# Kernel tuning notes

Measured on AMD Instinct MI355X. Metric: run time of the kernel, lower is better.

## Reference

```python
import jax, jax.numpy as jnp
from jax import lax
import numpy as np

B, T, I, H, L, O = 256, 512, 1, 256, 4, 1


def setup_inputs() -> dict:
    key = jax.random.key(0)
    ks = jax.random.split(key, 4 * L + 3)
    s = 1.0 / np.sqrt(H)
    inp = {"x": jax.random.normal(ks[0], (B, T, I), dtype=jnp.float32)}
    for l in range(L):
        in_dim = I if l == 0 else H
        inp[f"W_ih{l}"] = jax.random.uniform(ks[1 + 4 * l], (4 * H, in_dim), minval=-s, maxval=s, dtype=jnp.float32)
        inp[f"W_hh{l}"] = jax.random.uniform(ks[2 + 4 * l], (4 * H, H), minval=-s, maxval=s, dtype=jnp.float32)
        inp[f"b_ih{l}"] = jax.random.uniform(ks[3 + 4 * l], (4 * H,), minval=-s, maxval=s, dtype=jnp.float32)
        inp[f"b_hh{l}"] = jax.random.uniform(ks[4 + 4 * l], (4 * H,), minval=-s, maxval=s, dtype=jnp.float32)
    inp["fc_W"] = jax.random.uniform(ks[-2], (O, H), minval=-s, maxval=s, dtype=jnp.float32)
    inp["fc_b"] = jax.random.uniform(ks[-1], (O,), minval=-s, maxval=s, dtype=jnp.float32)
    return inp


def _lstm_layer(x_seq, W_ih, W_hh, b_ih, b_hh):
    # x_seq: [B, T, in_dim] -> hidden sequence [B, T, H]
    b, t = x_seq.shape[0], x_seq.shape[1]
    h = W_hh.shape[1]
    # precompute input projections for all timesteps: [T, B, 4H]
    xg = jnp.einsum('bti,gi->tbg', x_seq, W_ih) + b_ih + b_hh

    def step(carry, xg_t):
        hp, cp = carry
        gates = xg_t + hp @ W_hh.T  # [B, 4H]
        i, f, g, o = jnp.split(gates, 4, axis=-1)  # PyTorch gate order: i,f,g,o
        i = jax.nn.sigmoid(i)
        f = jax.nn.sigmoid(f)
        g = jnp.tanh(g)
        o = jax.nn.sigmoid(o)
        c = f * cp + i * g
        hn = o * jnp.tanh(c)
        return (hn, c), hn

    h0 = jnp.zeros((b, h), x_seq.dtype)
    _, hs = lax.scan(step, (h0, h0), xg)
    return jnp.transpose(hs, (1, 0, 2))  # [B, T, H]


def reference(x, W_ih0, W_hh0, b_ih0, b_hh0, W_ih1, W_hh1, b_ih1, b_hh1,
              W_ih2, W_hh2, b_ih2, b_hh2, W_ih3, W_hh3, b_ih3, b_hh3, fc_W, fc_b):
    layers = [(W_ih0, W_hh0, b_ih0, b_hh0), (W_ih1, W_hh1, b_ih1, b_hh1),
              (W_ih2, W_hh2, b_ih2, b_hh2), (W_ih3, W_hh3, b_ih3, b_hh3)]
    out = x
    for Wi, Wh, bi, bh in layers:
        out = _lstm_layer(out, Wi, Wh, bi, bh)
    # final linear on last timestep hidden: [B, H] -> [B, O]
    return out[:, -1, :] @ fc_W.T + fc_b
```

## Files before the change

kernel.cpp:

```cpp
#include <hip/hip_runtime.h>
#include <stdint.h>

#define T_ 512
#define H_ 256
#define MB 32
#define NBUF 8
#define ISLOT 8192
#define NWG 256

typedef __attribute__((ext_vector_type(8))) short  short8;
typedef __attribute__((ext_vector_type(4))) float  floatx4;
typedef __attribute__((ext_vector_type(4))) unsigned int uint4v;
typedef unsigned long long ull;

struct Params {
  const float* x;
  const float* Wih[4]; const float* Whh[4]; const float* bih[4]; const float* bhh[4];
  const float* fcW; const float* fcb;
  int*   flags;
  int*   xcd;
  short* hring;
};

__device__ __forceinline__ short f2bf(float f){
  uint32_t u = __builtin_bit_cast(uint32_t, f);
  u += 0x7fffu + ((u >> 16) & 1u);
  return (short)(u >> 16);
}
__device__ __forceinline__ float bf2f(short s){
  uint32_t u = ((uint32_t)(uint16_t)s) << 16;
  return __builtin_bit_cast(float, u);
}
__device__ __forceinline__ float sigm(float v){ return 1.0f / (1.0f + __expf(-v)); }
__device__ __forceinline__ float tanh_(float v){
  float a = fabsf(v);
  float e = __expf(-2.0f * a);
  float r = (1.0f - e) / (1.0f + e);
  return v < 0.0f ? -r : r;
}

__device__ __forceinline__ void a_st32(unsigned* p, unsigned v){
  __hip_atomic_store(p, v, __ATOMIC_RELAXED, __HIP_MEMORY_SCOPE_AGENT);
}
__device__ __forceinline__ int a_ldi(const int* p){
  return __hip_atomic_load(p, __ATOMIC_RELAXED, __HIP_MEMORY_SCOPE_AGENT);
}
__device__ __forceinline__ void a_sti(int* p, int v){
  __hip_atomic_store(p, v, __ATOMIC_RELAXED, __HIP_MEMORY_SCOPE_AGENT);
}

__device__ __forceinline__ int ctr_poll(const int* p){
  int v; int z = 0;
  asm volatile("global_atomic_add %0, %1, %2, off sc0\n\t"
               "s_waitcnt vmcnt(0)"
               : "=v"(v) : "v"(p), "v"(z) : "memory");
  return v;
}
__device__ __forceinline__ void ctr_post(int* p){
  int one = 1;
  asm volatile("global_atomic_add %0, %1, off" :: "v"(p), "v"(one) : "memory");
}

template<bool SL> __device__ __forceinline__ void ld16t(uint4v& d, const void* p){
  if constexpr (SL) asm volatile("global_load_dwordx4 %0, %1, off sc0 sc1" : "=v"(d) : "v"(p));
  else              asm volatile("global_load_dwordx4 %0, %1, off sc0"     : "=v"(d) : "v"(p));
}
template<bool SL> __device__ __forceinline__ void st32t(unsigned* p, unsigned v){
  if constexpr (SL) a_st32(p, v);
  else asm volatile("global_store_dword %0, %1, off sc0" :: "v"(p), "v"(v) : "memory");
}
typedef __attribute__((address_space(1))) const void as1void;
typedef __attribute__((address_space(3))) void       as3void;
__device__ __forceinline__ void gld_lds16(const void* g, void* l){
  __builtin_amdgcn_global_load_lds((as1void*)g, (as3void*)l, 16, 0, 1);
}
__device__ __forceinline__ void inv_l1(){
  asm volatile("buffer_inv sc0" ::: "memory");
}

__device__ __forceinline__ void ldf32(float& d, const void* p){
  asm volatile("global_load_dword %0, %1, off" : "=v"(d) : "v"(p));
}
template<int N> __device__ __forceinline__ void waitvm(){
  if constexpr (N == 0) asm volatile("s_waitcnt vmcnt(0)" ::: "memory");
  else if constexpr (N == 1) asm volatile("s_waitcnt vmcnt(1)" ::: "memory");
  else                       asm volatile("s_waitcnt vmcnt(4)" ::: "memory");
}
__device__ __forceinline__ void bar_lds(){
  asm volatile("s_waitcnt lgkmcnt(0)" ::: "memory");
  __builtin_amdgcn_s_barrier();
}
__device__ __forceinline__ void bar_only(){
  __builtin_amdgcn_s_barrier();
}

#define MFMA(a,b,c) __builtin_amdgcn_mfma_f32_16x16x32_bf16((a),(b),(c),0,0,0)

__device__ __forceinline__ void wpoll(const int* p, int thr, bool& dead){
  if (dead) return;
  int guard = 0;
  for (;;){
    int v = a_ldi(p);
    if (__all((int)(v >= thr))) break;
    if (++guard > (1 << 16)) { dead = true; break; }
  }
}

__device__ __forceinline__ void cpoll(const int* self, const int* up, const int* down,
                                      int t, bool& dead){
  if (dead) return;
  const int lane = threadIdx.x & 63;
  const int* p = nullptr; int thr = 0;
  if (lane == 0)            { p = self; thr = t; }
  else if (lane == 1 && up) { p = up;   thr = t + 2; }
  else if (lane == 2 && down && ((t & 3) == 0)){ p = down; thr = t - 4; }
  if (thr > T_) thr = T_;
  thr <<= 3;
  int guard = 0;
  for (;;){
    int v = p ? ctr_poll(p) : 0x7fffffff;
    if (__all((int)(v >= thr))) break;
    __builtin_amdgcn_s_sleep(1);
    if (++guard > (1 << 14)) { dead = true; break; }
  }
}

template<bool L0, bool SL>
__device__ __forceinline__ void run_cell(const Params& p, int g, int l, int slice,
    short* a_frag, float (*g_lds)[MB][34], float (*bias_lds)[32],
    float (*wih0_lds)[32], float* x0_lds)
{
  constexpr int KBT = L0 ? 8 : 16;
  const int tid = threadIdx.x, lane = tid & 63, wave = tid >> 6;
  const int n15 = lane & 15, q4 = lane >> 4;

  int* fl_self = p.flags + (g * 4 + l) * 32;
  int* fl_up   = L0 ? fl_self : fl_self - 32;
  int* fl_down = (l < 3) ? fl_self + 32 : fl_self;
  short* hr_self = p.hring + (size_t)((g * 4 + l) * NBUF) * ISLOT;
  const short* hr_up = L0 ? (const short*)nullptr
                          : hr_self - (size_t)NBUF * ISLOT;

  int* ctr_self = fl_self;
  const int* ctr_up   = L0 ? (const int*)nullptr : fl_self - 32;
  const int* ctr_down = (l < 3) ? fl_self + 32 : (const int*)nullptr;

  if (tid < 128){
    int gt = tid >> 5, j = tid & 31;
    int gr = gt * 256 + slice * 32 + j;
    bias_lds[gt][j] = p.bih[l][gr] + p.bhh[l][gr];
    if (L0) wih0_lds[gt][j] = p.Wih[0][gr];
  }

  short8 wf0[KBT], wf1[KBT];
  const int g0 = wave * 256 + slice * 32 + n15;
  const int g1 = g0 + 16;
  #pragma unroll
  for (int kb = 0; kb < KBT; ++kb){
    const float* base; int kk;
    if (L0)          { base = p.Whh[0]; kk = kb * 32 + q4 * 8; }
    else if (kb < 8) { base = p.Wih[l]; kk = kb * 32 + q4 * 8; }
    else             { base = p.Whh[l]; kk = (kb - 8) * 32 + q4 * 8; }
    const float* p0 = base + (size_t)g0 * H_ + kk;
    const float* p1 = base + (size_t)g1 * H_ + kk;
    short8 a, b;
    #pragma unroll
    for (int i = 0; i < 8; ++i){ a[i] = f2bf(p0[i]); b[i] = f2bf(p1[i]); }
    wf0[kb] = a; wf1[kb] = b;
  }

  float c00 = 0.f, c01 = 0.f, c10 = 0.f, c11 = 0.f;
  const int r0 = (tid >> 4) * 2, r1 = r0 + 1;
  const int pc = (tid & 15) * 2;

  const int* pp; int dlt;
  if (lane < 8)      { pp = fl_self + lane; dlt = 0; }
  else if (lane < 16){ if (L0){ pp = fl_self; dlt = -1000000; }
                       else   { pp = fl_up + (lane - 8); dlt = 2; } }
  else if (lane < 24){ if (l < 3){ pp = fl_down + (lane - 16); dlt = -7; }
                       else      { pp = fl_self; dlt = -1000000; } }
  else               { pp = fl_self + (lane & 7); dlt = -1000000; }
  bool dead = false;

  uint4v* fragv = (uint4v*)a_frag;
  uint4v px[4];
  float xcur = 0.f;

  if (!L0){
    if constexpr (SL){
      wpoll(fl_up + (lane & 7), 1, dead);
    } else {
      if (wave == 0) cpoll(ctr_self, ctr_up, ctr_down, -1, dead);
      __syncthreads();
      inv_l1();
    }
    const char* s = (const char*)hr_up;
    #pragma unroll
    for (int k = 0; k < 4; ++k) ld16t<SL>(px[k], s + (size_t)(k * 256 + tid) * 16);
  } else if (wave == 0 && lane < MB){
    ldf32(xcur, &p.x[(size_t)(g * MB + lane) * T_]);
  }
  waitvm<0>();
  __syncthreads();

  for (int t = 0; t < T_; ++t){
    const bool havh = (t > 0);
    const bool pf = (t + 1 < T_);
    const int hbase = L0 ? 0 : 1024;
    uint4v hv[4];
    floatx4 acc[2][2][2] = {};

    if constexpr (SL){
      { int thr = t + dlt; if (thr > T_) thr = T_;
        wpoll(pp, thr, dead); }
      if (!L0){
        #pragma unroll
        for (int k = 0; k < 4; ++k) fragv[k * 256 + tid] = px[k];
      } else if (wave == 0 && lane < MB){
        x0_lds[lane] = xcur;
      }
      if (havh){
        const char* s = (const char*)(hr_self + (size_t)((t - 1) & 7) * ISLOT);
        #pragma unroll
        for (int k = 0; k < 4; ++k) ld16t<SL>(hv[k], s + (size_t)(k * 256 + tid) * 16);
      }
      if (!L0){
        if (pf){
          const char* s = (const char*)(hr_up + (size_t)((t + 1) & 7) * ISLOT);
          #pragma unroll
          for (int k = 0; k < 4; ++k) ld16t<SL>(px[k], s + (size_t)(k * 256 + tid) * 16);
        }
      } else if (wave == 0 && lane < MB && pf){
        ldf32(xcur, &p.x[(size_t)(g * MB + lane) * T_ + (t + 1)]);
      }
      bar_lds();
      if (!L0){
        #pragma unroll
        for (int kb = 0; kb < 8; ++kb){
          #pragma unroll
          for (int mt = 0; mt < 2; ++mt){
            short8 af = *(short8*)&a_frag[(kb * 2 + mt) * 512 + lane * 8];
            int pr = kb & 1;
            acc[mt][0][pr] = MFMA(af, wf0[kb], acc[mt][0][pr]);
            acc[mt][1][pr] = MFMA(af, wf1[kb], acc[mt][1][pr]);
          }
        }
      }
      if (!L0){ if (pf) waitvm<4>(); else waitvm<0>(); }
      else    { if (wave == 0 && pf) waitvm<1>(); else waitvm<0>(); }
      if (havh){
        #pragma unroll
        for (int k = 0; k < 4; ++k) fragv[hbase + k * 256 + tid] = hv[k];
      } else {
        uint4v z = {0, 0, 0, 0};
        #pragma unroll
        for (int k = 0; k < 4; ++k) fragv[hbase + k * 256 + tid] = z;
      }
      bar_lds();
    } else if constexpr (!L0){
      #pragma unroll
      for (int k = 0; k < 4; ++k) fragv[k * 256 + tid] = px[k];
      bar_lds();
      #pragma unroll
      for (int kb = 0; kb < 4; ++kb){
        #pragma unroll
        for (int mt = 0; mt < 2; ++mt){
          short8 af = *(short8*)&a_frag[(kb * 2 + mt) * 512 + lane * 8];
          int pr = kb & 1;
          acc[mt][0][pr] = MFMA(af, wf0[kb], acc[mt][0][pr]);
          acc[mt][1][pr] = MFMA(af, wf1[kb], acc[mt][1][pr]);
        }
      }
      if (wave == 0) cpoll(ctr_self, ctr_up, ctr_down, t, dead);
      bar_only();
      inv_l1();
      if (havh){
        const char* s = (const char*)(hr_self + (size_t)((t - 1) & 7) * ISLOT);
        #pragma unroll
        for (int k = 0; k < 4; ++k){
          const char* src = s + (size_t)(k * 256 + tid) * 16;
          gld_lds16(src, (void*)&fragv[hbase + k * 256 + (tid & ~63)]);
        }
      }
      if (pf){
        const char* s = (const char*)(hr_up + (size_t)((t + 1) & 7) * ISLOT);
        #pragma unroll
        for (int k = 0; k < 4; ++k) ld16t<SL>(px[k], s + (size_t)(k * 256 + tid) * 16);
      }
      #pragma unroll
      for (int kb = 4; kb < 8; ++kb){
        #pragma unroll
        for (int mt = 0; mt < 2; ++mt){
          short8 af = *(short8*)&a_frag[(kb * 2 + mt) * 512 + lane * 8];
          int pr = kb & 1;
          acc[mt][0][pr] = MFMA(af, wf0[kb], acc[mt][0][pr]);
          acc[mt][1][pr] = MFMA(af, wf1[kb], acc[mt][1][pr]);
        }
      }
      if (pf) waitvm<4>(); else waitvm<0>();
      if (!havh){
        uint4v z = {0, 0, 0, 0};
        #pragma unroll
        for (int k = 0; k < 4; ++k) fragv[hbase + k * 256 + tid] = z;
      }
      bar_lds();
    } else {
      if (wave == 0) cpoll(ctr_self, ctr_up, ctr_down, t, dead);
      if (wave == 0 && lane < MB) x0_lds[lane] = xcur;
      bar_lds();
      inv_l1();
      if (havh){
        const char* s = (const char*)(hr_self + (size_t)((t - 1) & 7) * ISLOT);
        #pragma unroll
        for (int k = 0; k < 4; ++k){
          const char* src = s + (size_t)(k * 256 + tid) * 16;
          gld_lds16(src, (void*)&fragv[hbase + k * 256 + (tid & ~63)]);
        }
      }
      if (wave == 0 && lane < MB && pf){
        ldf32(xcur, &p.x[(size_t)(g * MB + lane) * T_ + (t + 1)]);
      }
      if (wave == 0 && pf) waitvm<1>(); else waitvm<0>();
      if (!havh){
        uint4v z = {0, 0, 0, 0};
        #pragma unroll
        for (int k = 0; k < 4; ++k) fragv[hbase + k * 256 + tid] = z;
      }
      bar_lds();
    }

    #pragma unroll
    for (int kb = (L0 ? 0 : 8); kb < KBT; ++kb){
      #pragma unroll
      for (int mt = 0; mt < 2; ++mt){
        short8 af = *(short8*)&a_frag[(kb * 2 + mt) * 512 + lane * 8];
        int pr = kb & 1;
        acc[mt][0][pr] = MFMA(af, wf0[kb], acc[mt][0][pr]);
        acc[mt][1][pr] = MFMA(af, wf1[kb], acc[mt][1][pr]);
      }
    }
    #pragma unroll
    for (int mt = 0; mt < 2; ++mt){
      floatx4 s0 = acc[mt][0][0] + acc[mt][0][1];
      floatx4 s1 = acc[mt][1][0] + acc[mt][1][1];
      int mrow = mt * 16 + q4 * 4;
      #pragma unroll
      for (int r = 0; r < 4; ++r){
        g_lds[wave][mrow + r][n15]      = s0[r];
        g_lds[wave][mrow + r][16 + n15] = s1[r];
      }
    }
    bar_lds();

    {
      float xs0 = 0.f, xs1 = 0.f;
      if (L0){ xs0 = x0_lds[r0]; xs1 = x0_lds[r1]; }
      float2 bi = *(const float2*)&bias_lds[0][pc];
      float2 bf = *(const float2*)&bias_lds[1][pc];
      float2 bg = *(const float2*)&bias_lds[2][pc];
      float2 bo = *(const float2*)&bias_lds[3][pc];
      float2 wi = {0.f,0.f}, wf = {0.f,0.f}, wg = {0.f,0.f}, wo = {0.f,0.f};
      if (L0){
        wi = *(const float2*)&wih0_lds[0][pc];
        wf = *(const float2*)&wih0_lds[1][pc];
        wg = *(const float2*)&wih0_lds[2][pc];
        wo = *(const float2*)&wih0_lds[3][pc];
      }
      short* slot = hr_self + (size_t)(t & 7) * ISLOT;
      #pragma unroll
      for (int rr = 0; rr < 2; ++rr){
        const int row = rr ? r1 : r0;
        const float xs = rr ? xs1 : xs0;
        float2 vi = *(const float2*)&g_lds[0][row][pc];
        float2 vf = *(const float2*)&g_lds[1][row][pc];
        float2 vg = *(const float2*)&g_lds[2][row][pc];
        float2 vo = *(const float2*)&g_lds[3][row][pc];
        float gi0 = vi.x + bi.x, gi1 = vi.y + bi.y;
        float gf0 = vf.x + bf.x, gf1 = vf.y + bf.y;
        float gg0 = vg.x + bg.x, gg1 = vg.y + bg.y;
        float go0 = vo.x + bo.x, go1 = vo.y + bo.y;
        if (L0){
          gi0 += xs * wi.x; gi1 += xs * wi.y;
          gf0 += xs * wf.x; gf1 += xs * wf.y;
          gg0 += xs * wg.x; gg1 += xs * wg.y;
          go0 += xs * wo.x; go1 += xs * wo.y;
        }
        float i0 = sigm(gi0), i1 = sigm(gi1);
        float f0 = sigm(gf0), f1 = sigm(gf1);
        float gv0 = tanh_(gg0), gv1 = tanh_(gg1);
        float o0 = sigm(go0), o1 = sigm(go1);
        float& ca = rr ? c10 : c00;
        float& cb = rr ? c11 : c01;
        ca = f0 * ca + i0 * gv0;
        cb = f1 * cb + i1 * gv1;
        float h0 = o0 * tanh_(ca);
        float h1 = o1 * tanh_(cb);
        unsigned pk = (unsigned)(uint16_t)f2bf(h0) | ((unsigned)(uint16_t)f2bf(h1) << 16);
        unsigned off = (unsigned)((slice * 2 + (row >> 4)) * 512
                     + ((pc >> 3) * 16 + (row & 15)) * 8 + (pc & 7));
        st32t<SL>((unsigned*)(slot + off), pk);
      }
    }

    waitvm<0>();
    bar_only();
    if (tid == 0){
      if constexpr (SL) a_sti(fl_self + slice, t + 1);
      else              ctr_post(ctr_self);
    }
  }
}

__global__ __launch_bounds__(256, 1) void lstm_kernel(Params p){
  __shared__ short a_frag[32 * 512];
  __shared__ float g_lds[4][MB][34];
  __shared__ float bias_lds[4][32];
  __shared__ float wih0_lds[4][32];
  __shared__ float x0_lds[MB];
  __shared__ int   fsh;

  const int bid   = blockIdx.x;
  const int g     = bid & 7;
  const int l     = (bid >> 3) & 3;
  const int slice = bid >> 5;

  int xcc;
  asm volatile("s_getreg_b32 %0, hwreg(HW_REG_XCC_ID)" : "=s"(xcc));
  const int me = xcc + 1;
  if (threadIdx.x == 0) a_sti(&p.xcd[bid], me);
  int fast;
  {
    const int lane = threadIdx.x & 63;
    const int idx = lane & 31;
    const int* xp = p.xcd + (idx >> 2) * 32 + (idx & 3) * 8 + g;
    int v = 0, guard = 0; bool giveup = false;
    for (;;){
      v = a_ldi(xp);
      if (__all((int)(v != 0))) break;
      if (++guard > (1 << 22)) { giveup = true; break; }
    }
    fast = (!giveup && __all((int)(v == me))) ? 1 : 0;
  }
  if (threadIdx.x == 0) fsh = 1;
  __syncthreads();
  if (!fast) fsh = 0;
  __syncthreads();
  fast = fsh;

  if (l == 0){
    if (fast) run_cell<true , false>(p, g, 0, slice, a_frag, g_lds, bias_lds, wih0_lds, x0_lds);
    else      run_cell<true , true >(p, g, 0, slice, a_frag, g_lds, bias_lds, wih0_lds, x0_lds);
  } else {
    if (fast) run_cell<false, false>(p, g, l, slice, a_frag, g_lds, bias_lds, wih0_lds, x0_lds);
    else      run_cell<false, true >(p, g, l, slice, a_frag, g_lds, bias_lds, wih0_lds, x0_lds);
  }
}

__global__ void fc_kernel(const short* __restrict__ hring, const float* __restrict__ fcW,
                          const float* __restrict__ fcb, float* __restrict__ out){
  int b = blockIdx.x, lane = threadIdx.x;
  int g = b >> 5, m = b & 31;
  int mt = m >> 4, mm = m & 15;
  const short* base = hring + (size_t)((g * 4 + 3) * NBUF + ((T_ - 1) & 7)) * ISLOT;
  float s = 0.f;
  #pragma unroll
  for (int k = 0; k < 4; ++k){
    int d = lane + 64 * k;
    int kb = d >> 5, koff = d & 31;
    short hv = base[(kb * 2 + mt) * 512 + ((koff >> 3) * 16 + mm) * 8 + (koff & 7)];
    s += bf2f(hv) * fcW[d];
  }
  #pragma unroll
  for (int off = 32; off; off >>= 1) s += __shfl_down(s, off);
  if (lane == 0) out[b] = s + fcb[0];
}

extern "C" void kernel_launch(void* const* d_in, const int* in_sizes, int n_in,
                              void* d_out, int out_size, void* d_ws, size_t ws_size,
                              hipStream_t stream) {
  Params P;
  P.x = (const float*)d_in[0];
  for (int l = 0; l < 4; ++l){
    P.Wih[l] = (const float*)d_in[1 + 4*l];
    P.Whh[l] = (const float*)d_in[2 + 4*l];
    P.bih[l] = (const float*)d_in[3 + 4*l];
    P.bhh[l] = (const float*)d_in[4 + 4*l];
  }
  P.fcW = (const float*)d_in[17];
  P.fcb = (const float*)d_in[18];

  char* ws = (char*)d_ws;
  P.flags = (int*)ws;
  P.xcd   = (int*)(ws + 4096);
  P.hring = (short*)(ws + 16384);

  hipMemsetAsync(ws, 0, 8192, stream);
  hipLaunchKernelGGL(lstm_kernel, dim3(NWG), dim3(256), 0, stream, P);
  hipLaunchKernelGGL(fc_kernel, dim3(256), dim3(64), 0, stream,
                     P.hring, P.fcW, P.fcb, (float*)d_out);
}
```

Before: 1.536 ms.

## Merge two hidden slices per workgroup and unify counter-based sync

New measurement: 6.027 ms. +292.4%, slower.

```diff
diff --git a/kernel.cpp b/kernel.cpp
--- a/kernel.cpp
+++ b/kernel.cpp
@@ -6,12 +6,12 @@
 #define MB 32
 #define NBUF 8
 #define ISLOT 8192
-#define NWG 256
+#define NWG 128
+#define NT 512
 
 typedef __attribute__((ext_vector_type(8))) short  short8;
 typedef __attribute__((ext_vector_type(4))) float  floatx4;
 typedef __attribute__((ext_vector_type(4))) unsigned int uint4v;
-typedef unsigned long long ull;
 
 struct Params {
   const float* x;
@@ -49,16 +49,26 @@
   __hip_atomic_store(p, v, __ATOMIC_RELAXED, __HIP_MEMORY_SCOPE_AGENT);
 }
 
-__device__ __forceinline__ int ctr_poll(const int* p){
+__device__ __forceinline__ int ctr_poll_l2(const int* p){
   int v; int z = 0;
   asm volatile("global_atomic_add %0, %1, %2, off sc0\n\t"
                "s_waitcnt vmcnt(0)"
                : "=v"(v) : "v"(p), "v"(z) : "memory");
   return v;
 }
-__device__ __forceinline__ void ctr_post(int* p){
+__device__ __forceinline__ void ctr_post_l2(int* p){
   int one = 1;
   asm volatile("global_atomic_add %0, %1, off" :: "v"(p), "v"(one) : "memory");
+}
+template<bool SL> __device__ __forceinline__ int ctr_sample(const int* p){
+  if constexpr (SL) return __hip_atomic_fetch_add((int*)p, 0, __ATOMIC_RELAXED,
+                                                  __HIP_MEMORY_SCOPE_AGENT);
+  else              return ctr_poll_l2(p);
+}
+template<bool SL> __device__ __forceinline__ void ctr_bump(int* p){
+  if constexpr (SL) (void)__hip_atomic_fetch_add(p, 1, __ATOMIC_RELAXED,
+                                                 __HIP_MEMORY_SCOPE_AGENT);
+  else              ctr_post_l2(p);
 }
 
 template<bool SL> __device__ __forceinline__ void ld16t(uint4v& d, const void* p){
@@ -81,10 +91,8 @@
 __device__ __forceinline__ void ldf32(float& d, const void* p){
   asm volatile("global_load_dword %0, %1, off" : "=v"(d) : "v"(p));
 }
-template<int N> __device__ __forceinline__ void waitvm(){
-  if constexpr (N == 0) asm volatile("s_waitcnt vmcnt(0)" ::: "memory");
-  else if constexpr (N == 1) asm volatile("s_waitcnt vmcnt(1)" ::: "memory");
-  else                       asm volatile("s_waitcnt vmcnt(4)" ::: "memory");
+__device__ __forceinline__ void waitvm0(){
+  asm volatile("s_waitcnt vmcnt(0)" ::: "memory");
 }
 __device__ __forceinline__ void bar_lds(){
   asm volatile("s_waitcnt lgkmcnt(0)" ::: "memory");
@@ -96,16 +104,7 @@
 
 #define MFMA(a,b,c) __builtin_amdgcn_mfma_f32_16x16x32_bf16((a),(b),(c),0,0,0)
 
-__device__ __forceinline__ void wpoll(const int* p, int thr, bool& dead){
-  if (dead) return;
-  int guard = 0;
-  for (;;){
-    int v = a_ldi(p);
-    if (__all((int)(v >= thr))) break;
-    if (++guard > (1 << 16)) { dead = true; break; }
-  }
-}
-
+template<bool SL>
 __device__ __forceinline__ void cpoll(const int* self, const int* up, const int* down,
                                       int t, bool& dead){
   if (dead) return;
@@ -115,10 +114,10 @@
   else if (lane == 1 && up) { p = up;   thr = t + 2; }
   else if (lane == 2 && down && ((t & 3) == 0)){ p = down; thr = t - 4; }
   if (thr > T_) thr = T_;
-  thr <<= 3;
+  thr <<= 2;
   int guard = 0;
   for (;;){
-    int v = p ? ctr_poll(p) : 0x7fffffff;
+    int v = p ? ctr_sample<SL>(p) : 0x7fffffff;
     if (__all((int)(v >= thr))) break;
     __builtin_amdgcn_s_sleep(1);
     if (++guard > (1 << 14)) { dead = true; break; }
@@ -126,34 +125,33 @@
 }
 
 template<bool L0, bool SL>
-__device__ __forceinline__ void run_cell(const Params& p, int g, int l, int slice,
-    short* a_frag, float (*g_lds)[MB][34], float (*bias_lds)[32],
-    float (*wih0_lds)[32], float* x0_lds)
+__device__ __forceinline__ void run_cell(const Params& p, int g, int l, int q,
+    short* a_frag, float (*g_lds)[4][MB][34], float (*bias_lds)[4][32],
+    float (*wih0_lds)[4][32], float* x0_lds)
 {
   constexpr int KBT = L0 ? 8 : 16;
   const int tid = threadIdx.x, lane = tid & 63, wave = tid >> 6;
+  const int sub = wave >> 2, gate = wave & 3;
+  const int slice = q * 2 + sub;
   const int n15 = lane & 15, q4 = lane >> 4;
-
-  int* fl_self = p.flags + (g * 4 + l) * 32;
-  int* fl_up   = L0 ? fl_self : fl_self - 32;
-  int* fl_down = (l < 3) ? fl_self + 32 : fl_self;
-  short* hr_self = p.hring + (size_t)((g * 4 + l) * NBUF) * ISLOT;
+  const int cell = g * 4 + l;
+
+  int* ctr_self = p.flags + cell * 32;
+  const int* ctr_up   = L0 ? (const int*)nullptr : ctr_self - 32;
+  const int* ctr_down = (l < 3) ? ctr_self + 32 : (const int*)nullptr;
+  short* hr_self = p.hring + (size_t)(cell * NBUF) * ISLOT;
   const short* hr_up = L0 ? (const short*)nullptr
                           : hr_self - (size_t)NBUF * ISLOT;
 
-  int* ctr_self = fl_self;
-  const int* ctr_up   = L0 ? (const int*)nullptr : fl_self - 32;
-  const int* ctr_down = (l < 3) ? fl_self + 32 : (const int*)nullptr;
-
-  if (tid < 128){
-    int gt = tid >> 5, j = tid & 31;
-    int gr = gt * 256 + slice * 32 + j;
-    bias_lds[gt][j] = p.bih[l][gr] + p.bhh[l][gr];
-    if (L0) wih0_lds[gt][j] = p.Wih[0][gr];
+  if (tid < 256){
+    int sb = tid >> 7, gt = (tid >> 5) & 3, j = tid & 31;
+    int gr = gt * 256 + (q * 2 + sb) * 32 + j;
+    bias_lds[sb][gt][j] = p.bih[l][gr] + p.bhh[l][gr];
+    if (L0) wih0_lds[sb][gt][j] = p.Wih[0][gr];
   }
 
   short8 wf0[KBT], wf1[KBT];
-  const int g0 = wave * 256 + slice * 32 + n15;
+  const int g0 = gate * 256 + slice * 32 + n15;
   const int g1 = g0 + 16;
   #pragma unroll
   for (int kb = 0; kb < KBT; ++kb){
@@ -170,96 +168,97 @@
   }
 
   float c00 = 0.f, c01 = 0.f, c10 = 0.f, c11 = 0.f;
-  const int r0 = (tid >> 4) * 2, r1 = r0 + 1;
-  const int pc = (tid & 15) * 2;
-
-  const int* pp; int dlt;
-  if (lane < 8)      { pp = fl_self + lane; dlt = 0; }
-  else if (lane < 16){ if (L0){ pp = fl_self; dlt = -1000000; }
-                       else   { pp = fl_up + (lane - 8); dlt = 2; } }
-  else if (lane < 24){ if (l < 3){ pp = fl_down + (lane - 16); dlt = -7; }
-                       else      { pp = fl_self; dlt = -1000000; } }
-  else               { pp = fl_self + (lane & 7); dlt = -1000000; }
+  const int sub_p = tid >> 8, st = tid & 255;
+  const int r0 = (st >> 4) * 2, r1 = r0 + 1;
+  const int pc = (st & 15) * 2;
+  const int slice_p = q * 2 + sub_p;
   bool dead = false;
 
   uint4v* fragv = (uint4v*)a_frag;
-  uint4v px[4];
+  uint4v px[2];
   float xcur = 0.f;
-
-  if (!L0){
-    if constexpr (SL){
-      wpoll(fl_up + (lane & 7), 1, dead);
-    } else {
-      if (wave == 0) cpoll(ctr_self, ctr_up, ctr_down, -1, dead);
-      __syncthreads();
-      inv_l1();
-    }
-    const char* s = (const char*)hr_up;
+  const int hbase = L0 ? 0 : 1024;
+
+  auto gates_out = [&](floatx4 (&acc)[2][2][2]){
     #pragma unroll
-    for (int k = 0; k < 4; ++k) ld16t<SL>(px[k], s + (size_t)(k * 256 + tid) * 16);
-  } else if (wave == 0 && lane < MB){
-    ldf32(xcur, &p.x[(size_t)(g * MB + lane) * T_]);
-  }
-  waitvm<0>();
-  __syncthreads();
-
-  for (int t = 0; t < T_; ++t){
-    const bool havh = (t > 0);
-    const bool pf = (t + 1 < T_);
-    const int hbase = L0 ? 0 : 1024;
-    uint4v hv[4];
-    floatx4 acc[2][2][2] = {};
-
-    if constexpr (SL){
-      { int thr = t + dlt; if (thr > T_) thr = T_;
-        wpoll(pp, thr, dead); }
-      if (!L0){
-        #pragma unroll
-        for (int k = 0; k < 4; ++k) fragv[k * 256 + tid] = px[k];
-      } else if (wave == 0 && lane < MB){
-        x0_lds[lane] = xcur;
-      }
-      if (havh){
-        const char* s = (const char*)(hr_self + (size_t)((t - 1) & 7) * ISLOT);
-        #pragma unroll
-        for (int k = 0; k < 4; ++k) ld16t<SL>(hv[k], s + (size_t)(k * 256 + tid) * 16);
-      }
-      if (!L0){
-        if (pf){
-          const char* s = (const char*)(hr_up + (size_t)((t + 1) & 7) * ISLOT);
-          #pragma unroll
-          for (int k = 0; k < 4; ++k) ld16t<SL>(px[k], s + (size_t)(k * 256 + tid) * 16);
-        }
-      } else if (wave == 0 && lane < MB && pf){
-        ldf32(xcur, &p.x[(size_t)(g * MB + lane) * T_ + (t + 1)]);
-      }
-      bar_lds();
-      if (!L0){
-        #pragma unroll
-        for (int kb = 0; kb < 8; ++kb){
-          #pragma unroll
-          for (int mt = 0; mt < 2; ++mt){
-            short8 af = *(short8*)&a_frag[(kb * 2 + mt) * 512 + lane * 8];
-            int pr = kb & 1;
-            acc[mt][0][pr] = MFMA(af, wf0[kb], acc[mt][0][pr]);
-            acc[mt][1][pr] = MFMA(af, wf1[kb], acc[mt][1][pr]);
-          }
-        }
-      }
-      if (!L0){ if (pf) waitvm<4>(); else waitvm<0>(); }
-      else    { if (wave == 0 && pf) waitvm<1>(); else waitvm<0>(); }
-      if (havh){
-        #pragma unroll
-        for (int k = 0; k < 4; ++k) fragv[hbase + k * 256 + tid] = hv[k];
-      } else {
-        uint4v z = {0, 0, 0, 0};
-        #pragma unroll
-        for (int k = 0; k < 4; ++k) fragv[hbase + k * 256 + tid] = z;
-      }
-      bar_lds();
-    } else if constexpr (!L0){
-      #pragma unroll
-      for (int k = 0; k < 4; ++k) fragv[k * 256 + tid] = px[k];
+    for (int mt = 0; mt < 2; ++mt){
+      floatx4 s0 = acc[mt][0][0] + acc[mt][0][1];
+      floatx4 s1 = acc[mt][1][0] + acc[mt][1][1];
+      int mrow = mt * 16 + q4 * 4;
+      #pragma unroll
+      for (int r = 0; r < 4; ++r){
+        g_lds[sub][gate][mrow + r][n15]      = s0[r];
+        g_lds[sub][gate][mrow + r][16 + n15] = s1[r];
+      }
+    }
+  };
+  auto pointwise = [&](int t){
+    float xs0 = 0.f, xs1 = 0.f;
+    if (L0){ xs0 = x0_lds[r0]; xs1 = x0_lds[r1]; }
+    float2 bi = *(const float2*)&bias_lds[sub_p][0][pc];
+    float2 bf = *(const float2*)&bias_lds[sub_p][1][pc];
+    float2 bg = *(const float2*)&bias_lds[sub_p][2][pc];
+    float2 bo = *(const float2*)&bias_lds[sub_p][3][pc];
+    float2 wi = {0.f,0.f}, wf = {0.f,0.f}, wg = {0.f,0.f}, wo = {0.f,0.f};
+    if (L0){
+      wi = *(const float2*)&wih0_lds[sub_p][0][pc];
+      wf = *(const float2*)&wih0_lds[sub_p][1][pc];
+      wg = *(const float2*)&wih0_lds[sub_p][2][pc];
+      wo = *(const float2*)&wih0_lds[sub_p][3][pc];
+    }
+    short* slot = hr_self + (size_t)(t & 7) * ISLOT;
+    #pragma unroll
+    for (int rr = 0; rr < 2; ++rr){
+      const int row = rr ? r1 : r0;
+      const float xs = rr ? xs1 : xs0;
+      float2 vi = *(const float2*)&g_lds[sub_p][0][row][pc];
+      float2 vf = *(const float2*)&g_lds[sub_p][1][row][pc];
+      float2 vg = *(const float2*)&g_lds[sub_p][2][row][pc];
+      float2 vo = *(const float2*)&g_lds[sub_p][3][row][pc];
+      float gi0 = vi.x + bi.x, gi1 = vi.y + bi.y;
+      float gf0 = vf.x + bf.x, gf1 = vf.y + bf.y;
+      float gg0 = vg.x + bg.x, gg1 = vg.y + bg.y;
+      float go0 = vo.x + bo.x, go1 = vo.y + bo.y;
+      if (L0){
+        gi0 += xs * wi.x; gi1 += xs * wi.y;
+        gf0 += xs * wf.x; gf1 += xs * wf.y;
+        gg0 += xs * wg.x; gg1 += xs * wg.y;
+        go0 += xs * wo.x; go1 += xs * wo.y;
+      }
+      float i0 = sigm(gi0), i1 = sigm(gi1);
+      float f0 = sigm(gf0), f1 = sigm(gf1);
+      float gv0 = tanh_(gg0), gv1 = tanh_(gg1);
+      float o0 = sigm(go0), o1 = sigm(go1);
+      float& ca = rr ? c10 : c00;
+      float& cb = rr ? c11 : c01;
+      ca = f0 * ca + i0 * gv0;
+      cb = f1 * cb + i1 * gv1;
+      float h0 = o0 * tanh_(ca);
+      float h1 = o1 * tanh_(cb);
+      unsigned pk = (unsigned)(uint16_t)f2bf(h0) | ((unsigned)(uint16_t)f2bf(h1) << 16);
+      unsigned off = (unsigned)((slice_p * 2 + (row >> 4)) * 512
+                   + ((pc >> 3) * 16 + (row & 15)) * 8 + (pc & 7));
+      st32t<SL>((unsigned*)(slot + off), pk);
+    }
+  };
+
+  if constexpr (!L0){
+    if (wave == 0) cpoll<SL>(ctr_self, ctr_up, ctr_down, -1, dead);
+    __syncthreads();
+    if constexpr (!SL) inv_l1();
+    { const char* s = (const char*)hr_up;
+      #pragma unroll
+      for (int k = 0; k < 2; ++k) ld16t<SL>(px[k], s + (size_t)(k * 512 + tid) * 16); }
+    waitvm0();
+    __syncthreads();
+
+    for (int t = 0; t < T_; ++t){
+      const bool havh = (t > 0);
+      const bool pf = (t + 1 < T_);
+      floatx4 acc[2][2][2] = {};
+      uint4v hv[2];
+      #pragma unroll
+      for (int k = 0; k < 2; ++k) fragv[k * 512 + tid] = px[k];
       bar_lds();
       #pragma unroll
       for (int kb = 0; kb < 4; ++kb){
@@ -271,21 +270,29 @@
           acc[mt][1][pr] = MFMA(af, wf1[kb], acc[mt][1][pr]);
         }
       }
-      if (wave == 0) cpoll(ctr_self, ctr_up, ctr_down, t, dead);
+      if (wave == 0) cpoll<SL>(ctr_self, ctr_up, ctr_down, t, dead);
       bar_only();
-      inv_l1();
-      if (havh){
-        const char* s = (const char*)(hr_self + (size_t)((t - 1) & 7) * ISLOT);
-        #pragma unroll
-        for (int k = 0; k < 4; ++k){
-          const char* src = s + (size_t)(k * 256 + tid) * 16;
-          gld_lds16(src, (void*)&fragv[hbase + k * 256 + (tid & ~63)]);
+      if constexpr (!SL){
+        inv_l1();
+        if (havh){
+          const char* s = (const char*)(hr_self + (size_t)((t - 1) & 7) * ISLOT);
+          #pragma unroll
+          for (int k = 0; k < 2; ++k){
+            const char* src = s + (size_t)(k * 512 + tid) * 16;
+            gld_lds16(src, (void*)&fragv[hbase + k * 512 + (tid & ~63)]);
+          }
+        }
+      } else {
+        if (havh){
+          const char* s = (const char*)(hr_self + (size_t)((t - 1) & 7) * ISLOT);
+          #pragma unroll
+          for (int k = 0; k < 2; ++k) ld16t<SL>(hv[k], s + (size_t)(k * 512 + tid) * 16);
         }
       }
       if (pf){
         const char* s = (const char*)(hr_up + (size_t)((t + 1) & 7) * ISLOT);
         #pragma unroll
-        for (int k = 0; k < 4; ++k) ld16t<SL>(px[k], s + (size_t)(k * 256 + tid) * 16);
+        for (int k = 0; k < 2; ++k) ld16t<SL>(px[k], s + (size_t)(k * 512 + tid) * 16);
       }
       #pragma unroll
       for (int kb = 4; kb < 8; ++kb){
@@ -297,132 +304,115 @@
           acc[mt][1][pr] = MFMA(af, wf1[kb], acc[mt][1][pr]);
         }
       }
-      if (pf) waitvm<4>(); else waitvm<0>();
+      waitvm0();
+      if constexpr (SL){
+        if (havh){
+          #pragma unroll
+          for (int k = 0; k < 2; ++k) fragv[hbase + k * 512 + tid] = hv[k];
+        }
+      }
       if (!havh){
         uint4v z = {0, 0, 0, 0};
         #pragma unroll
-        for (int k = 0; k < 4; ++k) fragv[hbase + k * 256 + tid] = z;
-      }
-      bar_lds();
-    } else {
-      if (wave == 0) cpoll(ctr_self, ctr_up, ctr_down, t, dead);
+        for (int k = 0; k < 2; ++k) fragv[hbase + k * 512 + tid] = z;
+      }
+      bar_lds();
+      #pragma unroll
+      for (int kb = 8; kb < 16; ++kb){
+        #pragma unroll
+        for (int mt = 0; mt < 2; ++mt){
+          short8 af = *(short8*)&a_frag[(kb * 2 + mt) * 512 + lane * 8];
+          int pr = kb & 1;
+          acc[mt][0][pr] = MFMA(af, wf0[kb], acc[mt][0][pr]);
+          acc[mt][1][pr] = MFMA(af, wf1[kb], acc[mt][1][pr]);
+        }
+      }
+      gates_out(acc);
+      bar_lds();
+      pointwise(t);
+      waitvm0();
+      bar_only();
+      if (tid == 0) ctr_bump<SL>(ctr_self);
+    }
+  } else {
+    if (wave == 0 && lane < MB) ldf32(xcur, &p.x[(size_t)(g * MB + lane) * T_]);
+    waitvm0();
+    __syncthreads();
+
+    for (int t = 0; t < T_; ++t){
+      const bool havh = (t > 0);
+      const bool pf = (t + 1 < T_);
+      floatx4 acc[2][2][2] = {};
+      uint4v hv[2];
+      if (wave == 0) cpoll<SL>(ctr_self, (const int*)nullptr, ctr_down, t, dead);
       if (wave == 0 && lane < MB) x0_lds[lane] = xcur;
       bar_lds();
-      inv_l1();
-      if (havh){
-        const char* s = (const char*)(hr_self + (size_t)((t - 1) & 7) * ISLOT);
-        #pragma unroll
-        for (int k = 0; k < 4; ++k){
-          const char* src = s + (size_t)(k * 256 + tid) * 16;
-          gld_lds16(src, (void*)&fragv[hbase + k * 256 + (tid & ~63)]);
+      if constexpr (!SL){
+        inv_l1();
+        if (havh){
+          const char* s = (const char*)(hr_self + (size_t)((t - 1) & 7) * ISLOT);
+          #pragma unroll
+          for (int k = 0; k < 2; ++k){
+            const char* src = s + (size_t)(k * 512 + tid) * 16;
+            gld_lds16(src, (void*)&fragv[hbase + k * 512 + (tid & ~63)]);
+          }
+        }
+      } else {
+        if (havh){
+          const char* s = (const char*)(hr_self + (size_t)((t - 1) & 7) * ISLOT);
+          #pragma unroll
+          for (int k = 0; k < 2; ++k) ld16t<SL>(hv[k], s + (size_t)(k * 512 + tid) * 16);
         }
       }
       if (wave == 0 && lane < MB && pf){
         ldf32(xcur, &p.x[(size_t)(g * MB + lane) * T_ + (t + 1)]);
       }
-      if (wave == 0 && pf) waitvm<1>(); else waitvm<0>();
+      waitvm0();
+      if constexpr (SL){
+        if (havh){
+          #pragma unroll
+          for (int k = 0; k < 2; ++k) fragv[hbase + k * 512 + tid] = hv[k];
+        }
+      }
       if (!havh){
         uint4v z = {0, 0, 0, 0};
         #pragma unroll
-        for (int k = 0; k < 4; ++k) fragv[hbase + k * 256 + tid] = z;
-      }
-      bar_lds();
-    }
-
-    #pragma unroll
-    for (int kb = (L0 ? 0 : 8); kb < KBT; ++kb){
-      #pragma unroll
-      for (int mt = 0; mt < 2; ++mt){
-        short8 af = *(short8*)&a_frag[(kb * 2 + mt) * 512 + lane * 8];
-        int pr = kb & 1;
-        acc[mt][0][pr] = MFMA(af, wf0[kb], acc[mt][0][pr]);
-        acc[mt][1][pr] = MFMA(af, wf1[kb], acc[mt][1][pr]);
-      }
-    }
-    #pragma unroll
-    for (int mt = 0; mt < 2; ++mt){
-      floatx4 s0 = acc[mt][0][0] + acc[mt][0][1];
-      floatx4 s1 = acc[mt][1][0] + acc[mt][1][1];
-      int mrow = mt * 16 + q4 * 4;
-      #pragma unroll
-      for (int r = 0; r < 4; ++r){
-        g_lds[wave][mrow + r][n15]      = s0[r];
-        g_lds[wave][mrow + r][16 + n15] = s1[r];
-      }
-    }
-    bar_lds();
-
-    {
-      float xs0 = 0.f, xs1 = 0.f;
-      if (L0){ xs0 = x0_lds[r0]; xs1 = x0_lds[r1]; }
-      float2 bi = *(const float2*)&bias_lds[0][pc];
-      float2 bf = *(const float2*)&bias_lds[1][pc];
-      float2 bg = *(const float2*)&bias_lds[2][pc];
-      float2 bo = *(const float2*)&bias_lds[3][pc];
-      float2 wi = {0.f,0.f}, wf = {0.f,0.f}, wg = {0.f,0.f}, wo = {0.f,0.f};
-      if (L0){
-        wi = *(const float2*)&wih0_lds[0][pc];
-        wf = *(const float2*)&wih0_lds[1][pc];
-        wg = *(const float2*)&wih0_lds[2][pc];
-        wo = *(const float2*)&wih0_lds[3][pc];
-      }
-      short* slot = hr_self + (size_t)(t & 7) * ISLOT;
-      #pragma unroll
-      for (int rr = 0; rr < 2; ++rr){
-        const int row = rr ? r1 : r0;
-        const float xs = rr ? xs1 : xs0;
-        float2 vi = *(const float2*)&g_lds[0][row][pc];
-        float2 vf = *(const float2*)&g_lds[1][row][pc];
-        float2 vg = *(const float2*)&g_lds[2][row][pc];
-        float2 vo = *(const float2*)&g_lds[3][row][pc];
-        float gi0 = vi.x + bi.x, gi1 = vi.y + bi.y;
-        float gf0 = vf.x + bf.x, gf1 = vf.y + bf.y;
-        float gg0 = vg.x + bg.x, gg1 = vg.y + bg.y;
-        float go0 = vo.x + bo.x, go1 = vo.y + bo.y;
-        if (L0){
-          gi0 += xs * wi.x; gi1 += xs * wi.y;
-          gf0 += xs * wf.x; gf1 += xs * wf.y;
-          gg0 += xs * wg.x; gg1 += xs * wg.y;
-          go0 += xs * wo.x; go1 += xs * wo.y;
-        }
-        float i0 = sigm(gi0), i1 = sigm(gi1);
-        float f0 = sigm(gf0), f1 = sigm(gf1);
-        float gv0 = tanh_(gg0), gv1 = tanh_(gg1);
-        float o0 = sigm(go0), o1 = sigm(go1);
-        float& ca = rr ? c10 : c00;
-        float& cb = rr ? c11 : c01;
-        ca = f0 * ca + i0 * gv0;
-        cb = f1 * cb + i1 * gv1;
-        float h0 = o0 * tanh_(ca);
-        float h1 = o1 * tanh_(cb);
-        unsigned pk = (unsigned)(uint16_t)f2bf(h0) | ((unsigned)(uint16_t)f2bf(h1) << 16);
-        unsigned off = (unsigned)((slice * 2 + (row >> 4)) * 512
-                     + ((pc >> 3) * 16 + (row & 15)) * 8 + (pc & 7));
-        st32t<SL>((unsigned*)(slot + off), pk);
-      }
-    }
-
-    waitvm<0>();
-    bar_only();
-    if (tid == 0){
-      if constexpr (SL) a_sti(fl_self + slice, t + 1);
-      else              ctr_post(ctr_self);
-    }
-  }
-}
-
-__global__ __launch_bounds__(256, 1) void lstm_kernel(Params p){
-  __shared__ short a_frag[32 * 512];
-  __shared__ float g_lds[4][MB][34];
-  __shared__ float bias_lds[4][32];
-  __shared__ float wih0_lds[4][32];
-  __shared__ float x0_lds[MB];
-  __shared__ int   fsh;
-
-  const int bid   = blockIdx.x;
-  const int g     = bid & 7;
-  const int l     = (bid >> 3) & 3;
-  const int slice = bid >> 5;
+        for (int k = 0; k < 2; ++k) fragv[hbase + k * 512 + tid] = z;
+      }
+      bar_lds();
+      #pragma unroll
+      for (int kb = 0; kb < 8; ++kb){
+        #pragma unroll
+        for (int mt = 0; mt < 2; ++mt){
+          short8 af = *(short8*)&a_frag[(kb * 2 + mt) * 512 + lane * 8];
+          int pr = kb & 1;
+          acc[mt][0][pr] = MFMA(af, wf0[kb], acc[mt][0][pr]);
+          acc[mt][1][pr] = MFMA(af, wf1[kb], acc[mt][1][pr]);
+        }
+      }
+      gates_out(acc);
+      bar_lds();
+      pointwise(t);
+      waitvm0();
+      bar_only();
+      if (tid == 0) ctr_bump<SL>(ctr_self);
+    }
+  }
+}
+
+__global__ __launch_bounds__(NT, 1) void lstm_kernel(Params p){
+  extern __shared__ char smem[];
+  short* a_frag                  = (short*)smem;
+  float (*g_lds)[4][MB][34]      = (float (*)[4][MB][34])(smem + 32768);
+  float (*bias_lds)[4][32]       = (float (*)[4][32])(smem + 67584);
+  float (*wih0_lds)[4][32]       = (float (*)[4][32])(smem + 68608);
+  float* x0_lds                  = (float*)(smem + 69632);
+  __shared__ int fsh;
+
+  const int bid = blockIdx.x;
+  const int g   = bid & 7;
+  const int l   = (bid >> 3) & 3;
+  const int q   = bid >> 5;
 
   int xcc;
   asm volatile("s_getreg_b32 %0, hwreg(HW_REG_XCC_ID)" : "=s"(xcc));
@@ -431,7 +421,7 @@
   int fast;
   {
     const int lane = threadIdx.x & 63;
-    const int idx = lane & 31;
+    const int idx = lane & 15;
     const int* xp = p.xcd + (idx >> 2) * 32 + (idx & 3) * 8 + g;
     int v = 0, guard = 0; bool giveup = false;
     for (;;){
@@ -448,11 +438,11 @@
   fast = fsh;
 
   if (l == 0){
-    if (fast) run_cell<true , false>(p, g, 0, slice, a_frag, g_lds, bias_lds, wih0_lds, x0_lds);
-    else      run_cell<true , true >(p, g, 0, slice, a_frag, g_lds, bias_lds, wih0_lds, x0_lds);
+    if (fast) run_cell<true , false>(p, g, 0, q, a_frag, g_lds, bias_lds, wih0_lds, x0_lds);
+    else      run_cell<true , true >(p, g, 0, q, a_frag, g_lds, bias_lds, wih0_lds, x0_lds);
   } else {
-    if (fast) run_cell<false, false>(p, g, l, slice, a_frag, g_lds, bias_lds, wih0_lds, x0_lds);
-    else      run_cell<false, true >(p, g, l, slice, a_frag, g_lds, bias_lds, wih0_lds, x0_lds);
+    if (fast) run_cell<false, false>(p, g, l, q, a_frag, g_lds, bias_lds, wih0_lds, x0_lds);
+    else      run_cell<false, true >(p, g, l, q, a_frag, g_lds, bias_lds, wih0_lds, x0_lds);
   }
 }
 
@@ -495,7 +485,7 @@
   P.hring = (short*)(ws + 16384);
 
   hipMemsetAsync(ws, 0, 8192, stream);
-  hipLaunchKernelGGL(lstm_kernel, dim3(NWG), dim3(256), 0, stream, P);
+  hipLaunchKernelGGL(lstm_kernel, dim3(NWG), dim3(NT), 69760, stream, P);
   hipLaunchKernelGGL(fc_kernel, dim3(256), dim3(64), 0, stream,
                      P.hring, P.fcW, P.fcb, (float*)d_out);
 }
```
